# Optimization experiments

Measured on AMD Instinct MI355X. Metric: run time of the kernel, lower is better.

Reference implementation:

```python
import jax, jax.numpy as jnp
import numpy as np

H = 512      # n_lstm_hidden (hardcoded in module)
ATTN = 256   # n_attn_hidden (hardcoded in module)


def setup_inputs() -> dict:
    key = jax.random.key(0)
    ks = jax.random.split(key, 10)
    seq_len, teams, nt = 16, 16, 64
    na = teams * 8
    bs = seq_len * nt
    return {
        "x": jax.random.normal(ks[0], (seq_len, teams, 16), jnp.float32),
        "hxs": jax.random.normal(ks[1], (bs, na, H), jnp.float32),
        "cxs": jax.random.normal(ks[2], (bs, na, H), jnp.float32),
        "h_self": jax.random.normal(ks[3], (bs, na, H), jnp.float32),
        "h_inter": jax.random.normal(ks[4], (bs, na, ATTN), jnp.float32),
        "reset": jax.random.randint(ks[5], (bs, 1), 0, 2, jnp.int32),
        "W_ih": jax.random.normal(ks[6], (4 * H, H), jnp.float32) * 0.02,
        "W_hh": jax.random.normal(ks[7], (4 * H, H), jnp.float32) * 0.02,
        "b_ih": jnp.zeros((4 * H,), jnp.float32),
        "b_hh": jnp.zeros((4 * H,), jnp.float32),
    }


def reference(x, hxs, cxs, h_self, h_inter, reset, W_ih, W_hh, b_ih, b_hh):
    seq_len, teams = x.shape[0], x.shape[1]
    na = teams * 8
    bs = h_self.shape[0]
    nt = bs // seq_len

    # LSTM input: tail half of self features concatenated with inter features -> (bs, na, H)
    h = jnp.concatenate([h_self[:, :, ATTN:], h_inter], axis=-1)
    # (bs, na, H) -> (seq_len, nt*na, H), matching view(nt,seq,na,-1).transpose(1,0)
    h_seq = h.reshape(nt, seq_len, na, H).transpose(1, 0, 2, 3).reshape(seq_len, nt * na, H)

    # per-step keep mask: resets[i::seq_len] == reset.reshape(nt, seq_len)[:, i]
    m = 1.0 - reset.astype(h.dtype).reshape(nt, seq_len).T          # (seq_len, nt)
    m_seq = jnp.broadcast_to(m[:, :, None], (seq_len, nt, na)).reshape(seq_len, nt * na, 1)

    # initial state from each trajectory start: hxs[::seq_len]
    h0 = hxs[::seq_len].reshape(nt * na, H)
    c0 = cxs[::seq_len].reshape(nt * na, H)

    def step(carry, inp):
        hp, cp = carry
        xt, mt = inp
        hp = hp * mt
        cp = cp * mt
        gates = xt @ W_ih.T + b_ih + hp @ W_hh.T + b_hh
        i, f, g, o = jnp.split(gates, 4, axis=-1)
        c = jax.nn.sigmoid(f) * cp + jax.nn.sigmoid(i) * jnp.tanh(g)
        hn = jax.nn.sigmoid(o) * jnp.tanh(c)
        return (hn, c), (hn, c)

    _, (hys, cys) = jax.lax.scan(step, (h0, c0), (h_seq, m_seq))

    def fold(y):
        # (seq_len, nt*na, H) -> transpose to (nt, seq, na, H) contiguous,
        # then torch .view(seq_len, nt, -1) reinterpretation == reshape here
        return y.reshape(seq_len, nt, na, H).transpose(1, 0, 2, 3).reshape(seq_len, nt, na * H)

    hys_out = fold(hys)
    cys_out = fold(cys)
    return (hys_out, cys_out)
```

## Files before the change

### kernel.cpp

```cpp
#include <hip/hip_runtime.h>

typedef __attribute__((ext_vector_type(8))) short bf16x8;
typedef __attribute__((ext_vector_type(8))) unsigned short u16x8;
typedef __attribute__((ext_vector_type(16))) float f32x16;

#define SEQ 16
#define NAG 128
#define HD  512

__device__ __forceinline__ unsigned short f2bf(float x) {
  unsigned int u = __float_as_uint(x);
  return (unsigned short)((u + 0x7fffu + ((u >> 16) & 1u)) >> 16);
}
__device__ __forceinline__ float sigm(float x) { return 1.0f / (1.0f + __expf(-x)); }
__device__ __forceinline__ float tanh_(float x) { return 2.0f / (1.0f + __expf(-2.0f * x)) - 1.0f; }

__global__ void prep_pack32(const float* __restrict__ Wih, const float* __restrict__ Whh,
                            const float* __restrict__ bih, const float* __restrict__ bhh,
                            unsigned short* __restrict__ Wpk, float* __restrict__ bsum) {
  const int t  = blockIdx.x >> 6;
  const int ks = blockIdx.x & 63;
  const int l  = threadIdx.x;
  const int n  = t * 32 + (l & 31);
  const int k  = ks * 16 + (l >> 5) * 8;
  const float* p = (k < 512) ? (Wih + (size_t)n * 512 + k) : (Whh + (size_t)n * 512 + (k - 512));
  float4 w0 = *(const float4*)p;
  float4 w1 = *(const float4*)(p + 4);
  bf16x8 v = {(short)f2bf(w0.x), (short)f2bf(w0.y), (short)f2bf(w0.z), (short)f2bf(w0.w),
              (short)f2bf(w1.x), (short)f2bf(w1.y), (short)f2bf(w1.z), (short)f2bf(w1.w)};
  *(bf16x8*)(Wpk + ((size_t)blockIdx.x * 64 + l) * 8) = v;
  if (ks == 0 && l < 32) bsum[n] = bih[n] + bhh[n];
}

__global__ __launch_bounds__(512, 1)
void lstm_step(const int t,
               const float* __restrict__ hxs, const float* __restrict__ cxs,
               const float* __restrict__ h_self, const float* __restrict__ h_inter,
               const int* __restrict__ reset,
               const unsigned short* __restrict__ Wpk, const float* __restrict__ bsum,
               float* out) {
  __shared__ __align__(16) unsigned short abuf[2][128 * 256];

  const int tid  = threadIdx.x;
  const int w    = tid >> 6;
  const int lane = tid & 63;
  const int c32  = lane & 31;
  const int kh   = lane >> 5;
  const int wr   = w >> 2;
  const int wc   = w & 3;

  const int bid  = blockIdx.x;
  const int ns   = bid & 3;
  const int traj = bid >> 2;
  const int b    = traj * SEQ + t;
  const int mt   = 1 - reset[b];
  const bool first = (t == 0);
  const size_t CYS = (size_t)SEQ * 64 * NAG * HD;

  const int rS = tid >> 2;
  const int q4 = tid & 3;

  auto stage = [&](int kc, int bufi) {
    unsigned short* dst = abuf[bufi];
    const int swr = (rS & 31) << 3;
    if (kc < 2) {
      const float* src = (kc == 0)
          ? h_self  + ((size_t)b * NAG + rS) * HD + 256
          : h_inter + ((size_t)b * NAG + rS) * 256;
      #pragma unroll
      for (int p = 0; p < 8; ++p) {
        int kl = q4 * 64 + p * 8;
        float4 v0 = *(const float4*)(src + kl);
        float4 v1 = *(const float4*)(src + kl + 4);
        u16x8 u = {f2bf(v0.x), f2bf(v0.y), f2bf(v0.z), f2bf(v0.w),
                   f2bf(v1.x), f2bf(v1.y), f2bf(v1.z), f2bf(v1.w)};
        *(u16x8*)&dst[rS * 256 + (kl ^ swr)] = u;
      }
    } else {
      const int hk0 = (kc - 2) * 256;
      const float* src = first
          ? hxs + ((size_t)b * NAG + rS) * HD + hk0
          : out + ((size_t)(b - 1) * NAG + rS) * HD + hk0;
      #pragma unroll
      for (int p = 0; p < 8; ++p) {
        int kl = q4 * 64 + p * 8;
        u16x8 u = {0, 0, 0, 0, 0, 0, 0, 0};
        if (mt) {
          float4 v0 = *(const float4*)(src + kl);
          float4 v1 = *(const float4*)(src + kl + 4);
          u = u16x8{f2bf(v0.x), f2bf(v0.y), f2bf(v0.z), f2bf(v0.w),
                    f2bf(v1.x), f2bf(v1.y), f2bf(v1.z), f2bf(v1.w)};
        }
        *(u16x8*)&dst[rS * 256 + (kl ^ swr)] = u;
      }
    }
  };

  const int hd = ns * 128 + wc * 32 + c32;
  f32x16 acc[2][4];
  #pragma unroll
  for (int q = 0; q < 4; ++q) {
    float bq = bsum[q * 512 + hd];
    #pragma unroll
    for (int rt = 0; rt < 2; ++rt)
      #pragma unroll
      for (int e = 0; e < 16; ++e) acc[rt][q][e] = bq;
  }

  const unsigned short* Wt[4];
  #pragma unroll
  for (int q = 0; q < 4; ++q) Wt[q] = Wpk + (size_t)(q * 16 + ns * 4 + wc) * 32768 + (size_t)lane * 8;

  bf16x8 Bq[2][4];
  auto ldB = [&](bf16x8* B, int ks) {
    const int off = ks * 512;
    B[0] = *(const bf16x8*)(Wt[0] + off);
    B[1] = *(const bf16x8*)(Wt[1] + off);
    B[2] = *(const bf16x8*)(Wt[2] + off);
    B[3] = *(const bf16x8*)(Wt[3] + off);
  };
  ldB(Bq[0], 0);
  ldB(Bq[1], 1);

  stage(0, 0);
  __syncthreads();

  const int swA = c32 << 3;
  const int arow0 = wr * 64 + c32;
  const int arow1 = wr * 64 + 32 + c32;

  #pragma unroll 1
  for (int kc = 0; kc < 4; ++kc) {
    if (kc < 3) stage(kc + 1, (kc + 1) & 1);
    const unsigned short* ab = abuf[kc & 1];
    #pragma unroll 1
    for (int k2 = 0; k2 < 8; ++k2) {
      {
        const int ksl = k2 * 2;
        const int kk = ksl * 16 + kh * 8;
        bf16x8 a0 = *(const bf16x8*)&ab[arow0 * 256 + (kk ^ swA)];
        bf16x8 a1 = *(const bf16x8*)&ab[arow1 * 256 + (kk ^ swA)];
        __builtin_amdgcn_s_setprio(1);
        acc[0][0] = __builtin_amdgcn_mfma_f32_32x32x16_bf16(a0, Bq[0][0], acc[0][0], 0, 0, 0);
        acc[0][1] = __builtin_amdgcn_mfma_f32_32x32x16_bf16(a0, Bq[0][1], acc[0][1], 0, 0, 0);
        acc[0][2] = __builtin_amdgcn_mfma_f32_32x32x16_bf16(a0, Bq[0][2], acc[0][2], 0, 0, 0);
        acc[0][3] = __builtin_amdgcn_mfma_f32_32x32x16_bf16(a0, Bq[0][3], acc[0][3], 0, 0, 0);
        acc[1][0] = __builtin_amdgcn_mfma_f32_32x32x16_bf16(a1, Bq[0][0], acc[1][0], 0, 0, 0);
        acc[1][1] = __builtin_amdgcn_mfma_f32_32x32x16_bf16(a1, Bq[0][1], acc[1][1], 0, 0, 0);
        acc[1][2] = __builtin_amdgcn_mfma_f32_32x32x16_bf16(a1, Bq[0][2], acc[1][2], 0, 0, 0);
        acc[1][3] = __builtin_amdgcn_mfma_f32_32x32x16_bf16(a1, Bq[0][3], acc[1][3], 0, 0, 0);
        __builtin_amdgcn_s_setprio(0);
        int kf = kc * 16 + ksl + 2;
        if (kf < 64) ldB(Bq[0], kf);
      }
      {
        const int ksl = k2 * 2 + 1;
        const int kk = ksl * 16 + kh * 8;
        bf16x8 a0 = *(const bf16x8*)&ab[arow0 * 256 + (kk ^ swA)];
        bf16x8 a1 = *(const bf16x8*)&ab[arow1 * 256 + (kk ^ swA)];
        __builtin_amdgcn_s_setprio(1);
        acc[0][0] = __builtin_amdgcn_mfma_f32_32x32x16_bf16(a0, Bq[1][0], acc[0][0], 0, 0, 0);
        acc[0][1] = __builtin_amdgcn_mfma_f32_32x32x16_bf16(a0, Bq[1][1], acc[0][1], 0, 0, 0);
        acc[0][2] = __builtin_amdgcn_mfma_f32_32x32x16_bf16(a0, Bq[1][2], acc[0][2], 0, 0, 0);
        acc[0][3] = __builtin_amdgcn_mfma_f32_32x32x16_bf16(a0, Bq[1][3], acc[0][3], 0, 0, 0);
        acc[1][0] = __builtin_amdgcn_mfma_f32_32x32x16_bf16(a1, Bq[1][0], acc[1][0], 0, 0, 0);
        acc[1][1] = __builtin_amdgcn_mfma_f32_32x32x16_bf16(a1, Bq[1][1], acc[1][1], 0, 0, 0);
        acc[1][2] = __builtin_amdgcn_mfma_f32_32x32x16_bf16(a1, Bq[1][2], acc[1][2], 0, 0, 0);
        acc[1][3] = __builtin_amdgcn_mfma_f32_32x32x16_bf16(a1, Bq[1][3], acc[1][3], 0, 0, 0);
        __builtin_amdgcn_s_setprio(0);
        int kf = kc * 16 + ksl + 2;
        if (kf < 64) ldB(Bq[1], kf);
      }
    }
    __syncthreads();
  }

  #pragma unroll
  for (int rt = 0; rt < 2; ++rt) {
    #pragma unroll
    for (int reg = 0; reg < 16; ++reg) {
      const int arow = wr * 64 + rt * 32 + ((reg & 3) + 8 * (reg >> 2) + 4 * kh);
      float cp;
      if (first) cp = cxs[((size_t)b * NAG + arow) * HD + hd];
      else       cp = out[CYS + ((size_t)(b - 1) * NAG + arow) * HD + hd];
      cp = mt ? cp : 0.0f;
      float gi = acc[rt][0][reg];
      float gf = acc[rt][1][reg];
      float gg = acc[rt][2][reg];
      float go = acc[rt][3][reg];
      float cn = sigm(gf) * cp + sigm(gi) * tanh_(gg);
      float hn = sigm(go) * tanh_(cn);
      const size_t ob = ((size_t)b * NAG + arow) * HD + hd;
      out[ob] = hn;
      out[CYS + ob] = cn;
    }
  }
}

__device__ __forceinline__ bf16x8 loadBf(const float* __restrict__ Wih,
                                         const float* __restrict__ Whh,
                                         int tile, int ks, int lane) {
  int n = tile * 32 + (lane & 31);
  int k = ks * 16 + (lane >> 5) * 8;
  const float* p = (k < 512) ? (Wih + (size_t)n * 512 + k) : (Whh + (size_t)n * 512 + (k - 512));
  float4 w0 = *(const float4*)p;
  float4 w1 = *(const float4*)(p + 4);
  return bf16x8{(short)f2bf(w0.x), (short)f2bf(w0.y), (short)f2bf(w0.z), (short)f2bf(w0.w),
                (short)f2bf(w1.x), (short)f2bf(w1.y), (short)f2bf(w1.z), (short)f2bf(w1.w)};
}

__global__ __launch_bounds__(512, 2)
void lstm_fb(const float* __restrict__ hxs, const float* __restrict__ cxs,
             const float* __restrict__ h_self, const float* __restrict__ h_inter,
             const int* __restrict__ reset,
             const float* __restrict__ Wih, const float* __restrict__ Whh,
             const float* __restrict__ bih, const float* __restrict__ bhh,
             float* __restrict__ out) {
  __shared__ __align__(16) unsigned short x_lds[32 * 512];
  __shared__ __align__(16) unsigned short h_lds[2][32 * 512];
  const int tid = threadIdx.x;
  const int w = tid >> 6, lane = tid & 63;
  const int colB = lane & 31, khB = lane >> 5, row = colB;
  const int asw = (row & 7) << 3;
  const int bid = blockIdx.x, traj = bid >> 2, agent0 = (bid & 3) * 32;
  const int rS = tid >> 4, l16 = tid & 15, swS = (rS & 7) << 3;
  const size_t CYS = (size_t)SEQ * 64 * NAG * HD;
  {
    const float* src = hxs + ((size_t)traj * SEQ * NAG + (agent0 + rS)) * HD;
    #pragma unroll
    for (int p = 0; p < 8; ++p) {
      int k = p * 64 + l16 * 4;
      float4 v = *(const float4*)(src + k);
      *(ushort4*)&h_lds[0][rS * 512 + (k ^ swS)] =
          make_ushort4(f2bf(v.x), f2bf(v.y), f2bf(v.z), f2bf(v.w));
    }
  }
  float c_reg[2][16];
  float biasv[2][4];
  {
    #pragma unroll
    for (int u = 0; u < 2; ++u)
      #pragma unroll
      for (int q = 0; q < 4; ++q) {
        int n = q * 512 + w * 64 + u * 32 + colB;
        biasv[u][q] = bih[n] + bhh[n];
      }
    const size_t cbase = ((size_t)traj * SEQ * NAG + agent0) * HD;
    #pragma unroll
    for (int u = 0; u < 2; ++u)
      #pragma unroll
      for (int reg = 0; reg < 16; ++reg) {
        int r = (reg & 3) + 8 * (reg >> 2) + 4 * khB;
        c_reg[u][reg] = cxs[cbase + (size_t)r * HD + w * 64 + u * 32 + colB];
      }
  }
  for (int t = 0; t < SEQ; ++t) {
    const int b = traj * SEQ + t;
    const int mt = 1 - reset[b];
    const unsigned short* hcur = h_lds[t & 1];
    unsigned short* hnxt = h_lds[(t & 1) ^ 1];
    {
      const float* srcs = h_self + ((size_t)b * NAG + (agent0 + rS)) * HD + 256;
      const float* srci = h_inter + ((size_t)b * NAG + (agent0 + rS)) * 256;
      #pragma unroll
      for (int p = 0; p < 8; ++p) {
        int k = p * 64 + l16 * 4;
        const float* sp = (k < 256) ? (srcs + k) : (srci + (k - 256));
        float4 v = *(const float4*)sp;
        *(ushort4*)&x_lds[rS * 512 + (k ^ swS)] =
            make_ushort4(f2bf(v.x), f2bf(v.y), f2bf(v.z), f2bf(v.w));
      }
      if (mt == 0) {
        uint4* pz = (uint4*)h_lds[t & 1];
        #pragma unroll
        for (int i = 0; i < 4; ++i) pz[tid + i * 512] = uint4{0, 0, 0, 0};
      }
    }
    __syncthreads();
    auto lda = [&](int ks, const unsigned short* src) -> bf16x8 {
      int kk = (ks & 31) * 16 + khB * 8;
      return *(const bf16x8*)(src + row * 512 + (kk ^ asw));
    };
    #pragma unroll
    for (int u = 0; u < 2; ++u) {
      const int t0 = w * 2 + u, t1 = 16 + w * 2 + u, t2 = 32 + w * 2 + u, t3 = 48 + w * 2 + u;
      f32x16 acc[4];
      #pragma unroll
      for (int q = 0; q < 4; ++q)
        #pragma unroll
        for (int e = 0; e < 16; ++e) acc[q][e] = biasv[u][q];
      bf16x8 Ba[4], Bb[4];
      auto ldB = [&](bf16x8* B, int ks) {
        B[0] = loadBf(Wih, Whh, t0, ks, lane);
        B[1] = loadBf(Wih, Whh, t1, ks, lane);
        B[2] = loadBf(Wih, Whh, t2, ks, lane);
        B[3] = loadBf(Wih, Whh, t3, ks, lane);
      };
      ldB(Ba, 0);
      ldB(Bb, 1);
      #pragma unroll 1
      for (int kp = 0; kp < 32; ++kp) {
        const int ks0 = kp * 2;
        const unsigned short* ab = (ks0 < 32) ? x_lds : hcur;
        bf16x8 a0 = lda(ks0, ab);
        __builtin_amdgcn_s_setprio(1);
        acc[0] = __builtin_amdgcn_mfma_f32_32x32x16_bf16(a0, Ba[0], acc[0], 0, 0, 0);
        acc[1] = __builtin_amdgcn_mfma_f32_32x32x16_bf16(a0, Ba[1], acc[1], 0, 0, 0);
        acc[2] = __builtin_amdgcn_mfma_f32_32x32x16_bf16(a0, Ba[2], acc[2], 0, 0, 0);
        acc[3] = __builtin_amdgcn_mfma_f32_32x32x16_bf16(a0, Ba[3], acc[3], 0, 0, 0);
        __builtin_amdgcn_s_setprio(0);
        ldB(Ba, (ks0 + 2 < 64) ? ks0 + 2 : 63);
        const unsigned short* ab1 = (ks0 + 1 < 32) ? x_lds : hcur;
        bf16x8 a1 = lda(ks0 + 1, ab1);
        __builtin_amdgcn_s_setprio(1);
        acc[0] = __builtin_amdgcn_mfma_f32_32x32x16_bf16(a1, Bb[0], acc[0], 0, 0, 0);
        acc[1] = __builtin_amdgcn_mfma_f32_32x32x16_bf16(a1, Bb[1], acc[1], 0, 0, 0);
        acc[2] = __builtin_amdgcn_mfma_f32_32x32x16_bf16(a1, Bb[2], acc[2], 0, 0, 0);
        acc[3] = __builtin_amdgcn_mfma_f32_32x32x16_bf16(a1, Bb[3], acc[3], 0, 0, 0);
        __builtin_amdgcn_s_setprio(0);
        ldB(Bb, (ks0 + 3 < 64) ? ks0 + 3 : 63);
      }
      const int hd = w * 64 + u * 32 + colB;
      #pragma unroll
      for (int reg = 0; reg < 16; ++reg) {
        float gi = acc[0][reg], gf = acc[1][reg], gg = acc[2][reg], go = acc[3][reg];
        float cp = mt ? c_reg[u][reg] : 0.0f;
        float cn = sigm(gf) * cp + sigm(gi) * tanh_(gg);
        float hn = sigm(go) * tanh_(cn);
        c_reg[u][reg] = cn;
        int r = (reg & 3) + 8 * (reg >> 2) + 4 * khB;
        size_t ob = ((size_t)b * NAG + agent0 + r) * HD + hd;
        out[ob] = hn;
        out[CYS + ob] = cn;
        hnxt[r * 512 + (hd ^ ((r & 7) << 3))] = f2bf(hn);
      }
    }
    __syncthreads();
  }
}

extern "C" void kernel_launch(void* const* d_in, const int* in_sizes, int n_in,
                              void* d_out, int out_size, void* d_ws, size_t ws_size,
                              hipStream_t stream) {
  (void)in_sizes; (void)n_in; (void)out_size;
  const float* hxs     = (const float*)d_in[1];
  const float* cxs     = (const float*)d_in[2];
  const float* h_self  = (const float*)d_in[3];
  const float* h_inter = (const float*)d_in[4];
  const int*   reset   = (const int*)d_in[5];
  const float* Wih     = (const float*)d_in[6];
  const float* Whh     = (const float*)d_in[7];
  const float* bih     = (const float*)d_in[8];
  const float* bhh     = (const float*)d_in[9];
  float* out = (float*)d_out;

  const size_t needW = (size_t)2048 * 1024 * sizeof(unsigned short);
  const size_t need  = needW + 8192;

  if (d_ws != nullptr && ws_size >= need) {
    unsigned short* Wpk  = (unsigned short*)d_ws;
    float*          bsum = (float*)((char*)d_ws + needW);
    prep_pack32<<<4096, 64, 0, stream>>>(Wih, Whh, bih, bhh, Wpk, bsum);
    for (int t = 0; t < SEQ; ++t)
      lstm_step<<<256, 512, 0, stream>>>(t, hxs, cxs, h_self, h_inter, reset,
                                         Wpk, bsum, out);
  } else {
    lstm_fb<<<256, 512, 0, stream>>>(hxs, cxs, h_self, h_inter, reset,
                                     Wih, Whh, bih, bhh, out);
  }
}
```

Measured before the change: 1.093 ms.

## Precast LSTM inputs to bf16, add bf16 hidden ping-pong, halve per-block rows

A new pre-pass converts the concatenated self/inter features for all steps to bf16 once. Each step kernel now stages a full 64x1024 bf16 A tile into LDS in one shot, reading the previous hidden state from a bf16 ping-pong buffer instead of fp32 output. The grid doubles to 512 blocks with 64 rows each, so every wave does one row tile and four gate MFMAs per k-step. This removes per-step fp32 loads and conversions and in-loop barriers, at the cost of extra workspace, an extra bf16 store per output, and reading the weights twice as often per row.

```diff
diff --git a/kernel.cpp b/kernel.cpp
--- a/kernel.cpp
+++ b/kernel.cpp
@@ -4,9 +4,10 @@
 typedef __attribute__((ext_vector_type(8))) unsigned short u16x8;
 typedef __attribute__((ext_vector_type(16))) float f32x16;
 
-#define SEQ 16
-#define NAG 128
-#define HD  512
+#define SEQ   16
+#define NAG   128
+#define HD    512
+#define NTRAJ 64
 
 __device__ __forceinline__ unsigned short f2bf(float x) {
   unsigned int u = __float_as_uint(x);
@@ -32,86 +33,110 @@
   if (ks == 0 && l < 32) bsum[n] = bih[n] + bhh[n];
 }
 
+__global__ void prep_xbf(const float* __restrict__ h_self, const float* __restrict__ h_inter,
+                         unsigned short* __restrict__ xb) {
+  const int b   = blockIdx.x;
+  const int tid = threadIdx.x;
+  const int row = tid >> 1;
+  const int half = tid & 1;
+  const float* src = half
+      ? h_inter + ((size_t)b * NAG + row) * 256 - 256
+      : h_self  + ((size_t)b * NAG + row) * HD + 256;
+  unsigned short* dst = xb + ((size_t)b * NAG + row) * 512;
+  #pragma unroll
+  for (int p = 0; p < 32; ++p) {
+    int k = half * 256 + p * 8;
+    const float* sp = half ? (src + k) : (src + (k));
+    float4 v0 = *(const float4*)sp;
+    float4 v1 = *(const float4*)(sp + 4);
+    u16x8 u = {f2bf(v0.x), f2bf(v0.y), f2bf(v0.z), f2bf(v0.w),
+               f2bf(v1.x), f2bf(v1.y), f2bf(v1.z), f2bf(v1.w)};
+    *(u16x8*)&dst[k] = u;
+  }
+}
+
 __global__ __launch_bounds__(512, 1)
 void lstm_step(const int t,
                const float* __restrict__ hxs, const float* __restrict__ cxs,
-               const float* __restrict__ h_self, const float* __restrict__ h_inter,
                const int* __restrict__ reset,
                const unsigned short* __restrict__ Wpk, const float* __restrict__ bsum,
+               const unsigned short* __restrict__ xb, unsigned short* hping,
                float* out) {
-  __shared__ __align__(16) unsigned short abuf[2][128 * 256];
+  __shared__ __align__(16) unsigned short A[64 * 1024];
 
   const int tid  = threadIdx.x;
   const int w    = tid >> 6;
   const int lane = tid & 63;
   const int c32  = lane & 31;
   const int kh   = lane >> 5;
-  const int wr   = w >> 2;
-  const int wc   = w & 3;
+  const int rg   = w & 1;
+  const int ctq  = w >> 1;
 
   const int bid  = blockIdx.x;
   const int ns   = bid & 3;
-  const int traj = bid >> 2;
+  const int rb   = bid >> 2;
+  const int traj = rb >> 1;
+  const int row0 = (rb & 1) * 64;
   const int b    = traj * SEQ + t;
   const int mt   = 1 - reset[b];
-  const bool first = (t == 0);
-  const size_t CYS = (size_t)SEQ * 64 * NAG * HD;
-
-  const int rS = tid >> 2;
-  const int q4 = tid & 3;
-
-  auto stage = [&](int kc, int bufi) {
-    unsigned short* dst = abuf[bufi];
-    const int swr = (rS & 31) << 3;
-    if (kc < 2) {
-      const float* src = (kc == 0)
-          ? h_self  + ((size_t)b * NAG + rS) * HD + 256
-          : h_inter + ((size_t)b * NAG + rS) * 256;
-      #pragma unroll
-      for (int p = 0; p < 8; ++p) {
-        int kl = q4 * 64 + p * 8;
-        float4 v0 = *(const float4*)(src + kl);
-        float4 v1 = *(const float4*)(src + kl + 4);
-        u16x8 u = {f2bf(v0.x), f2bf(v0.y), f2bf(v0.z), f2bf(v0.w),
-                   f2bf(v1.x), f2bf(v1.y), f2bf(v1.z), f2bf(v1.w)};
-        *(u16x8*)&dst[rS * 256 + (kl ^ swr)] = u;
-      }
-    } else {
-      const int hk0 = (kc - 2) * 256;
-      const float* src = first
-          ? hxs + ((size_t)b * NAG + rS) * HD + hk0
-          : out + ((size_t)(b - 1) * NAG + rS) * HD + hk0;
-      #pragma unroll
-      for (int p = 0; p < 8; ++p) {
-        int kl = q4 * 64 + p * 8;
+  const size_t CYS = (size_t)SEQ * NTRAJ * NAG * HD;
+
+  {
+    const int r    = tid >> 3;
+    const int k8   = tid & 7;
+    const int grow = row0 + r;
+    const int sw   = (r & 31) << 3;
+    if (k8 < 4) {
+      const unsigned short* xsrc = xb + ((size_t)b * NAG + grow) * 512;
+      #pragma unroll
+      for (int p = 0; p < 16; ++p) {
+        int k = k8 * 128 + p * 8;
+        u16x8 v = *(const u16x8*)&xsrc[k];
+        *(u16x8*)&A[r * 1024 + (k ^ sw)] = v;
+      }
+    } else if (t == 0) {
+      const float* hsrc = hxs + ((size_t)b * NAG + grow) * HD;
+      #pragma unroll
+      for (int p = 0; p < 16; ++p) {
+        int k = k8 * 128 + p * 8;
+        int hk = k - 512;
         u16x8 u = {0, 0, 0, 0, 0, 0, 0, 0};
         if (mt) {
-          float4 v0 = *(const float4*)(src + kl);
-          float4 v1 = *(const float4*)(src + kl + 4);
+          float4 v0 = *(const float4*)(hsrc + hk);
+          float4 v1 = *(const float4*)(hsrc + hk + 4);
           u = u16x8{f2bf(v0.x), f2bf(v0.y), f2bf(v0.z), f2bf(v0.w),
                     f2bf(v1.x), f2bf(v1.y), f2bf(v1.z), f2bf(v1.w)};
         }
-        *(u16x8*)&dst[rS * 256 + (kl ^ swr)] = u;
-      }
-    }
-  };
-
-  const int hd = ns * 128 + wc * 32 + c32;
-  f32x16 acc[2][4];
+        *(u16x8*)&A[r * 1024 + (k ^ sw)] = u;
+      }
+    } else {
+      const unsigned short* hsrc =
+          hping + ((size_t)(((t - 1) & 1) * NTRAJ + traj) * NAG + grow) * 512;
+      #pragma unroll
+      for (int p = 0; p < 16; ++p) {
+        int k = k8 * 128 + p * 8;
+        u16x8 u = {0, 0, 0, 0, 0, 0, 0, 0};
+        if (mt) u = *(const u16x8*)&hsrc[k - 512];
+        *(u16x8*)&A[r * 1024 + (k ^ sw)] = u;
+      }
+    }
+  }
+
+  const int hd = ns * 128 + ctq * 32 + c32;
+  f32x16 acc[4];
   #pragma unroll
   for (int q = 0; q < 4; ++q) {
     float bq = bsum[q * 512 + hd];
     #pragma unroll
-    for (int rt = 0; rt < 2; ++rt)
-      #pragma unroll
-      for (int e = 0; e < 16; ++e) acc[rt][q][e] = bq;
+    for (int e = 0; e < 16; ++e) acc[q][e] = bq;
   }
 
   const unsigned short* Wt[4];
   #pragma unroll
-  for (int q = 0; q < 4; ++q) Wt[q] = Wpk + (size_t)(q * 16 + ns * 4 + wc) * 32768 + (size_t)lane * 8;
-
-  bf16x8 Bq[2][4];
+  for (int q = 0; q < 4; ++q)
+    Wt[q] = Wpk + (size_t)(q * 16 + ns * 4 + ctq) * 32768 + (size_t)lane * 8;
+
+  bf16x8 B0[4], B1[4];
   auto ldB = [&](bf16x8* B, int ks) {
     const int off = ks * 512;
     B[0] = *(const bf16x8*)(Wt[0] + off);
@@ -119,81 +144,57 @@
     B[2] = *(const bf16x8*)(Wt[2] + off);
     B[3] = *(const bf16x8*)(Wt[3] + off);
   };
-  ldB(Bq[0], 0);
-  ldB(Bq[1], 1);
-
-  stage(0, 0);
+  ldB(B0, 0);
+  ldB(B1, 1);
+
   __syncthreads();
 
-  const int swA = c32 << 3;
-  const int arow0 = wr * 64 + c32;
-  const int arow1 = wr * 64 + 32 + c32;
+  const int arow = rg * 32 + c32;
+  const int asw  = c32 << 3;
 
   #pragma unroll 1
-  for (int kc = 0; kc < 4; ++kc) {
-    if (kc < 3) stage(kc + 1, (kc + 1) & 1);
-    const unsigned short* ab = abuf[kc & 1];
-    #pragma unroll 1
-    for (int k2 = 0; k2 < 8; ++k2) {
-      {
-        const int ksl = k2 * 2;
-        const int kk = ksl * 16 + kh * 8;
-        bf16x8 a0 = *(const bf16x8*)&ab[arow0 * 256 + (kk ^ swA)];
-        bf16x8 a1 = *(const bf16x8*)&ab[arow1 * 256 + (kk ^ swA)];
-        __builtin_amdgcn_s_setprio(1);
-        acc[0][0] = __builtin_amdgcn_mfma_f32_32x32x16_bf16(a0, Bq[0][0], acc[0][0], 0, 0, 0);
-        acc[0][1] = __builtin_amdgcn_mfma_f32_32x32x16_bf16(a0, Bq[0][1], acc[0][1], 0, 0, 0);
-        acc[0][2] = __builtin_amdgcn_mfma_f32_32x32x16_bf16(a0, Bq[0][2], acc[0][2], 0, 0, 0);
-        acc[0][3] = __builtin_amdgcn_mfma_f32_32x32x16_bf16(a0, Bq[0][3], acc[0][3], 0, 0, 0);
-        acc[1][0] = __builtin_amdgcn_mfma_f32_32x32x16_bf16(a1, Bq[0][0], acc[1][0], 0, 0, 0);
-        acc[1][1] = __builtin_amdgcn_mfma_f32_32x32x16_bf16(a1, Bq[0][1], acc[1][1], 0, 0, 0);
-        acc[1][2] = __builtin_amdgcn_mfma_f32_32x32x16_bf16(a1, Bq[0][2], acc[1][2], 0, 0, 0);
-        acc[1][3] = __builtin_amdgcn_mfma_f32_32x32x16_bf16(a1, Bq[0][3], acc[1][3], 0, 0, 0);
-        __builtin_amdgcn_s_setprio(0);
-        int kf = kc * 16 + ksl + 2;
-        if (kf < 64) ldB(Bq[0], kf);
-      }
-      {
-        const int ksl = k2 * 2 + 1;
-        const int kk = ksl * 16 + kh * 8;
-        bf16x8 a0 = *(const bf16x8*)&ab[arow0 * 256 + (kk ^ swA)];
-        bf16x8 a1 = *(const bf16x8*)&ab[arow1 * 256 + (kk ^ swA)];
-        __builtin_amdgcn_s_setprio(1);
-        acc[0][0] = __builtin_amdgcn_mfma_f32_32x32x16_bf16(a0, Bq[1][0], acc[0][0], 0, 0, 0);
-        acc[0][1] = __builtin_amdgcn_mfma_f32_32x32x16_bf16(a0, Bq[1][1], acc[0][1], 0, 0, 0);
-        acc[0][2] = __builtin_amdgcn_mfma_f32_32x32x16_bf16(a0, Bq[1][2], acc[0][2], 0, 0, 0);
-        acc[0][3] = __builtin_amdgcn_mfma_f32_32x32x16_bf16(a0, Bq[1][3], acc[0][3], 0, 0, 0);
-        acc[1][0] = __builtin_amdgcn_mfma_f32_32x32x16_bf16(a1, Bq[1][0], acc[1][0], 0, 0, 0);
-        acc[1][1] = __builtin_amdgcn_mfma_f32_32x32x16_bf16(a1, Bq[1][1], acc[1][1], 0, 0, 0);
-        acc[1][2] = __builtin_amdgcn_mfma_f32_32x32x16_bf16(a1, Bq[1][2], acc[1][2], 0, 0, 0);
-        acc[1][3] = __builtin_amdgcn_mfma_f32_32x32x16_bf16(a1, Bq[1][3], acc[1][3], 0, 0, 0);
-        __builtin_amdgcn_s_setprio(0);
-        int kf = kc * 16 + ksl + 2;
-        if (kf < 64) ldB(Bq[1], kf);
-      }
-    }
-    __syncthreads();
-  }
-
+  for (int kp = 0; kp < 32; ++kp) {
+    const int ks0 = kp * 2;
+    {
+      bf16x8 a = *(const bf16x8*)&A[arow * 1024 + ((ks0 * 16 + kh * 8) ^ asw)];
+      __builtin_amdgcn_s_setprio(1);
+      acc[0] = __builtin_amdgcn_mfma_f32_32x32x16_bf16(a, B0[0], acc[0], 0, 0, 0);
+      acc[1] = __builtin_amdgcn_mfma_f32_32x32x16_bf16(a, B0[1], acc[1], 0, 0, 0);
+      acc[2] = __builtin_amdgcn_mfma_f32_32x32x16_bf16(a, B0[2], acc[2], 0, 0, 0);
+      acc[3] = __builtin_amdgcn_mfma_f32_32x32x16_bf16(a, B0[3], acc[3], 0, 0, 0);
+      __builtin_amdgcn_s_setprio(0);
+      ldB(B0, (ks0 + 2 < 64) ? ks0 + 2 : 63);
+    }
+    {
+      bf16x8 a = *(const bf16x8*)&A[arow * 1024 + (((ks0 + 1) * 16 + kh * 8) ^ asw)];
+      __builtin_amdgcn_s_setprio(1);
+      acc[0] = __builtin_amdgcn_mfma_f32_32x32x16_bf16(a, B1[0], acc[0], 0, 0, 0);
+      acc[1] = __builtin_amdgcn_mfma_f32_32x32x16_bf16(a, B1[1], acc[1], 0, 0, 0);
+      acc[2] = __builtin_amdgcn_mfma_f32_32x32x16_bf16(a, B1[2], acc[2], 0, 0, 0);
+      acc[3] = __builtin_amdgcn_mfma_f32_32x32x16_bf16(a, B1[3], acc[3], 0, 0, 0);
+      __builtin_amdgcn_s_setprio(0);
+      ldB(B1, (ks0 + 3 < 64) ? ks0 + 3 : 63);
+    }
+  }
+
+  unsigned short* hw = hping + ((size_t)((t & 1) * NTRAJ + traj) * NAG) * 512;
   #pragma unroll
-  for (int rt = 0; rt < 2; ++rt) {
-    #pragma unroll
-    for (int reg = 0; reg < 16; ++reg) {
-      const int arow = wr * 64 + rt * 32 + ((reg & 3) + 8 * (reg >> 2) + 4 * kh);
-      float cp;
-      if (first) cp = cxs[((size_t)b * NAG + arow) * HD + hd];
-      else       cp = out[CYS + ((size_t)(b - 1) * NAG + arow) * HD + hd];
-      cp = mt ? cp : 0.0f;
-      float gi = acc[rt][0][reg];
-      float gf = acc[rt][1][reg];
-      float gg = acc[rt][2][reg];
-      float go = acc[rt][3][reg];
-      float cn = sigm(gf) * cp + sigm(gi) * tanh_(gg);
-      float hn = sigm(go) * tanh_(cn);
-      const size_t ob = ((size_t)b * NAG + arow) * HD + hd;
-      out[ob] = hn;
-      out[CYS + ob] = cn;
-    }
+  for (int reg = 0; reg < 16; ++reg) {
+    const int crow = (reg & 3) + 8 * (reg >> 2) + 4 * kh;
+    const int grow = row0 + rg * 32 + crow;
+    float cp = (t == 0) ? cxs[((size_t)b * NAG + grow) * HD + hd]
+                        : out[CYS + ((size_t)(b - 1) * NAG + grow) * HD + hd];
+    cp = mt ? cp : 0.0f;
+    float gi = acc[0][reg];
+    float gf = acc[1][reg];
+    float gg = acc[2][reg];
+    float go = acc[3][reg];
+    float cn = sigm(gf) * cp + sigm(gi) * tanh_(gg);
+    float hn = sigm(go) * tanh_(cn);
+    const size_t ob = ((size_t)b * NAG + grow) * HD + hd;
+    out[ob] = hn;
+    out[CYS + ob] = cn;
+    hw[(size_t)grow * 512 + hd] = f2bf(hn);
   }
 }
 
@@ -224,7 +225,7 @@
   const int asw = (row & 7) << 3;
   const int bid = blockIdx.x, traj = bid >> 2, agent0 = (bid & 3) * 32;
   const int rS = tid >> 4, l16 = tid & 15, swS = (rS & 7) << 3;
-  const size_t CYS = (size_t)SEQ * 64 * NAG * HD;
+  const size_t CYS = (size_t)SEQ * NAG * NTRAJ * HD;
   {
     const float* src = hxs + ((size_t)traj * SEQ * NAG + (agent0 + rS)) * HD;
     #pragma unroll
@@ -354,16 +355,22 @@
   const float* bhh     = (const float*)d_in[9];
   float* out = (float*)d_out;
 
-  const size_t needW = (size_t)2048 * 1024 * sizeof(unsigned short);
-  const size_t need  = needW + 8192;
+  const size_t WPK_SZ  = (size_t)2048 * 1024 * 2;
+  const size_t BSUM_SZ = 8192;
+  const size_t XB_SZ   = (size_t)1024 * NAG * 512 * 2;
+  const size_t HP_SZ   = (size_t)2 * NTRAJ * NAG * 512 * 2;
+  const size_t need    = WPK_SZ + BSUM_SZ + XB_SZ + HP_SZ;
 
   if (d_ws != nullptr && ws_size >= need) {
-    unsigned short* Wpk  = (unsigned short*)d_ws;
-    float*          bsum = (float*)((char*)d_ws + needW);
+    char* base = (char*)d_ws;
+    unsigned short* Wpk   = (unsigned short*)base;
+    float*          bsum  = (float*)(base + WPK_SZ);
+    unsigned short* xb    = (unsigned short*)(base + WPK_SZ + BSUM_SZ);
+    unsigned short* hping = (unsigned short*)(base + WPK_SZ + BSUM_SZ + XB_SZ);
     prep_pack32<<<4096, 64, 0, stream>>>(Wih, Whh, bih, bhh, Wpk, bsum);
+    prep_xbf<<<1024, 256, 0, stream>>>(h_self, h_inter, xb);
     for (int t = 0; t < SEQ; ++t)
-      lstm_step<<<256, 512, 0, stream>>>(t, hxs, cxs, h_self, h_inter, reset,
-                                         Wpk, bsum, out);
+      lstm_step<<<512, 512, 0, stream>>>(t, hxs, cxs, reset, Wpk, bsum, xb, hping, out);
   } else {
     lstm_fb<<<256, 512, 0, stream>>>(hxs, cxs, h_self, h_inter, reset,
                                      Wih, Whh, bih, bhh, out);
```

Result: slower. 1.269 ms (+16.1%).
